# Kernel tuning notes

Hardware: AMD Instinct MI355X
Metric: run time of the kernel (lower is better)

Reference implementation:

```python
import jax, jax.numpy as jnp
import numpy as np

NUM_HEADS = 8
DIM = 256
NUM_Q = 1


def setup_inputs() -> dict:
    key = jax.random.key(0)
    ks = jax.random.split(key, 10)
    B, H, W, C = 4, 56, 56, DIM
    mask_h = mask_w = 7
    WinNum = mask_h * mask_w
    x = jax.random.normal(ks[0], (B, H, W, C), dtype=jnp.float32)
    clstoken = jax.random.normal(ks[1], (B, NUM_Q, C), dtype=jnp.float32)
    mask = jax.random.bernoulli(ks[2], 0.3, (B, WinNum, WinNum))
    # ensure each window attends to itself (avoid fully-masked rows)
    eye = jnp.eye(WinNum, dtype=bool)[None]
    mask = jnp.logical_or(mask, eye)
    Wqkv = jax.random.normal(ks[3], (C, 3 * C), dtype=jnp.float32) * (C ** -0.5)
    bqkv = jnp.zeros((3 * C,), dtype=jnp.float32)
    Wo = jax.random.normal(ks[4], (C, C), dtype=jnp.float32) * (C ** -0.5)
    bo = jnp.zeros((C,), dtype=jnp.float32)
    lepe_k = jax.random.normal(ks[5], (3, 3, 1, C), dtype=jnp.float32) * 0.1  # depthwise HWIO
    lepe_b = jnp.zeros((C,), dtype=jnp.float32)
    return {"x": x, "clstoken": clstoken, "mask": mask, "mask_h": mask_h,
            "mask_w": mask_w, "Wqkv": Wqkv, "bqkv": bqkv, "Wo": Wo, "bo": bo,
            "lepe_k": lepe_k, "lepe_b": lepe_b}


def _forward(x, clstoken, mask, mask_h, mask_w, Wqkv, bqkv, Wo, bo, lepe_k, lepe_b):
    B, H, W, C = x.shape
    num_q = clstoken.shape[1]
    Nh = NUM_HEADS
    Hd = C // Nh
    Win_h, Win_w = H // mask_h, W // mask_w
    WinPix = Win_h * Win_w
    WinNum = mask_h * mask_w
    L_win = H * W
    scale = C ** -0.5

    qkv = x @ Wqkv + bqkv                       # [B,H,W,3C]
    q, k, v = jnp.split(qkv, 3, axis=-1)
    qkv_cls = clstoken @ Wqkv + bqkv            # [B,Q,3C]
    q_cls, k_cls, v_cls = jnp.split(qkv_cls, 3, axis=-1)

    # depthwise lepe conv on v (NHWC)
    lepe = jax.lax.conv_general_dilated(
        v, lepe_k, window_strides=(1, 1), padding='SAME',
        dimension_numbers=('NHWC', 'HWIO', 'NHWC'), feature_group_count=C) + lepe_b

    def to_win(t):  # b (j h)(i w)(Nh Hd) -> b Nh (j i h w) Hd
        t = t.reshape(B, mask_h, Win_h, mask_w, Win_w, Nh, Hd)
        t = t.transpose(0, 5, 1, 3, 2, 4, 6)
        return t.reshape(B, Nh, L_win, Hd)

    def cls_heads(t):  # b q (Nh Hd) -> b Nh q Hd
        return t.reshape(B, num_q, Nh, Hd).transpose(0, 2, 1, 3)

    q_all = jnp.concatenate([to_win(q), cls_heads(q_cls)], axis=2)
    k_all = jnp.concatenate([to_win(k), cls_heads(k_cls)], axis=2)
    v_all = jnp.concatenate([to_win(v), cls_heads(v_cls)], axis=2)

    # token-level block mask; cls block (id WinNum) is globally visible
    blk = jnp.concatenate([jnp.arange(L_win) // WinPix,
                           jnp.full((num_q,), WinNum)])
    mask_ext = jnp.pad(mask, ((0, 0), (0, 1), (0, 1)), constant_values=True)
    tok_mask = mask_ext[:, blk[:, None], blk[None, :]]  # [B,L,L]

    scores = jnp.einsum('bnqd,bnkd->bnqk', q_all, k_all) * scale
    neg = jnp.finfo(scores.dtype).min
    scores = jnp.where(tok_mask[:, None], scores, neg)
    attn = jax.nn.softmax(scores, axis=-1)
    out = jnp.einsum('bnqk,bnkd->bnqd', attn, v_all)   # [B,Nh,L,Hd]

    cls_out = out[:, :, -num_q:, :]
    x_out = out[:, :, :-num_q, :]
    # b Nh (j i h w) Hd -> b (j h)(i w)(Nh Hd)
    x_out = x_out.reshape(B, Nh, mask_h, mask_w, Win_h, Win_w, Hd)
    x_out = x_out.transpose(0, 2, 4, 3, 5, 1, 6).reshape(B, H, W, C)
    cls_out = cls_out.transpose(0, 2, 1, 3).reshape(B, num_q, C)

    x_out = (x_out + lepe) @ Wo + bo
    cls_out = cls_out @ Wo + bo
    return x_out, cls_out


def reference(x, clstoken, mask, mask_h, mask_w, Wqkv, bqkv, Wo, bo, lepe_k, lepe_b):
    return _forward(x, clstoken, mask, mask_h, mask_w, Wqkv, bqkv, Wo, bo, lepe_k, lepe_b)
```

## Files before the change

kernel.cpp:

```cpp
#include <hip/hip_runtime.h>
#include <math.h>

#define B_      4
#define NH      8
#define HD      32
#define WINNUM  49
#define LWIN    3136
#define NTOK    3137
#define NPIX    12544
#define MROWS   12548
#define SCALE_L2E 0.09016844005556021f
#define SM_BIAS   4.0f

typedef _Float16 half_t;
using half8 = __attribute__((ext_vector_type(8))) half_t;
using half4 = __attribute__((ext_vector_type(4))) half_t;
using f32x4 = __attribute__((ext_vector_type(4))) float;

__device__ __forceinline__ unsigned pack2(float a, float b) {
    auto h = __builtin_amdgcn_cvt_pkrtz(a, b);
    return __builtin_bit_cast(unsigned, h);
}
__device__ __forceinline__ half8 as_h8(int4 v) {
    return __builtin_bit_cast(half8, v);
}

__global__ __launch_bounds__(256)
void prep(const float* __restrict__ x, const float* __restrict__ cls,
          const float* __restrict__ Wqkv, const float* __restrict__ Wo,
          half_t* __restrict__ xh, half_t* __restrict__ Wqkvt, half_t* __restrict__ Wot)
{
    const int idx = blockIdx.x * 256 + threadIdx.x;
    const int stride = gridDim.x * 256;
    for (int i = idx; i < MROWS * 256; i += stride) {
        int row = i >> 8, c = i & 255;
        float v = (row < NPIX) ? x[i] : cls[(row - NPIX) * 256 + c];
        xh[i] = (half_t)v;
    }
    for (int i = idx; i < 768 * 256; i += stride) {
        int n = i >> 8, k = i & 255;
        Wqkvt[i] = (half_t)Wqkv[k * 768 + n];
    }
    for (int i = idx; i < 256 * 256; i += stride) {
        int n = i >> 8, k = i & 255;
        Wot[i] = (half_t)Wo[k * 256 + n];
    }
}

__global__ __launch_bounds__(256)
void qkv_gemm(const half_t* __restrict__ xh, const half_t* __restrict__ Bt,
              const float* __restrict__ bqkv,
              half_t* __restrict__ qh, half_t* __restrict__ kh,
              half_t* __restrict__ khcls, half_t* __restrict__ vh,
              half_t* __restrict__ vplain)
{
    __shared__ __align__(16) short As[2][128 * 40];
    __shared__ __align__(16) short Bs[2][128 * 40];
    const int m0 = blockIdx.y * 128, n0 = blockIdx.x * 128;
    const int tid = threadIdx.x;
    const int lane = tid & 63, wv = tid >> 6;
    const int wm = wv >> 1, wn = wv & 1;
    const int qi = lane & 15, g = lane >> 4;
    f32x4 acc[4][4] = {};

    int4 ra[2], rb[2];
    auto issue = [&](int k0) {
#pragma unroll
        for (int i = 0; i < 2; ++i) {
            int ch = tid + 256 * i;
            int row = ch >> 2, kc = (ch & 3) * 8;
            int m = m0 + row;
            ra[i] = (m < MROWS) ? *(const int4*)(xh + (size_t)m * 256 + k0 + kc)
                                : make_int4(0, 0, 0, 0);
            rb[i] = *(const int4*)(Bt + (size_t)(n0 + row) * 256 + k0 + kc);
        }
    };
    auto commit = [&](int bu) {
#pragma unroll
        for (int i = 0; i < 2; ++i) {
            int ch = tid + 256 * i;
            int row = ch >> 2, kc = (ch & 3) * 8;
            *(int4*)&As[bu][row * 40 + kc] = ra[i];
            *(int4*)&Bs[bu][row * 40 + kc] = rb[i];
        }
    };

    issue(0); commit(0);
    __syncthreads();
    int buf = 0;
    for (int s = 0; s < 8; ++s) {
        if (s < 7) issue((s + 1) * 32);
        half8 af[4], bf[4];
#pragma unroll
        for (int f = 0; f < 4; ++f) {
            af[f] = *(const half8*)&As[buf][(wm * 64 + f * 16 + qi) * 40 + g * 8];
            bf[f] = *(const half8*)&Bs[buf][(wn * 64 + f * 16 + qi) * 40 + g * 8];
        }
#pragma unroll
        for (int fm = 0; fm < 4; ++fm)
#pragma unroll
            for (int fn = 0; fn < 4; ++fn)
                acc[fm][fn] = __builtin_amdgcn_mfma_f32_16x16x32_f16(af[fm], bf[fn], acc[fm][fn], 0, 0, 0);
        if (s < 7) commit(buf ^ 1);
        __syncthreads();
        buf ^= 1;
    }

    const int part = n0 >> 8;
    int nhv[4], dv[4];
    float bq[4];
#pragma unroll
    for (int fn = 0; fn < 4; ++fn) {
        int n = n0 + wn * 64 + fn * 16 + qi;
        bq[fn] = bqkv[n];
        int c = n & 255;
        nhv[fn] = c >> 5; dv[fn] = c & 31;
    }
#pragma unroll
    for (int fm = 0; fm < 4; ++fm) {
#pragma unroll
        for (int r = 0; r < 4; ++r) {
            int m = m0 + wm * 64 + fm * 16 + g * 4 + r;
            if (m >= MROWS) continue;
            int b, tok;
            if (m < NPIX) {
                b = m / LWIN;
                int p = m - b * LWIN;
                int hh = p / 56, ww = p - hh * 56;
                tok = ((hh >> 3) * 7 + (ww >> 3)) * 64 + ((hh & 7) << 3) + (ww & 7);
            } else { b = m - NPIX; tok = LWIN; }
#pragma unroll
            for (int fn = 0; fn < 4; ++fn) {
                float val = acc[fm][fn][r] + bq[fn];
                size_t bh = (size_t)(b * NH + nhv[fn]);
                int d = dv[fn];
                if (part == 0) {
                    qh[(bh * NTOK + tok) * 32 + d] = (half_t)(val * SCALE_L2E);
                } else if (part == 1) {
                    if (tok < LWIN) kh[(bh * WINNUM + (tok >> 6)) * 2560 + (tok & 63) * 40 + d] = (half_t)val;
                    else            khcls[bh * 32 + d] = (half_t)val;
                } else {
                    vplain[(bh * NTOK + tok) * 32 + d] = (half_t)val;
                    if (tok < LWIN) vh[(bh * WINNUM + (tok >> 6)) * 2560 + d * 80 + (tok & 63)] = (half_t)val;
                }
            }
        }
    }
}

__global__ __launch_bounds__(256)
void win_attn(const half_t* __restrict__ qh, const half_t* __restrict__ kh,
              const half_t* __restrict__ khcls, const half_t* __restrict__ vh,
              const half_t* __restrict__ vplain, const int* __restrict__ mask,
              half_t* __restrict__ tg, float* __restrict__ clspart)
{
    const int id = blockIdx.x;
    const int tid = threadIdx.x;
    __shared__ __align__(16) short Plds[4][16 * 72];
    __shared__ float redc[4 * 33];
    const int lane = tid & 63, wv = tid >> 6;

    if (id >= 1568) {
        const int cid = id - 1568;
        const int bh = cid >> 3;
        const int chunk = cid & 7;
        const int wstart = chunk * 6;
        const int nw = (chunk < 7) ? 6 : 7;
        const int nkeys = nw * 64;

        float q[32];
        {
            const half_t* qp = qh + ((size_t)bh * NTOK + LWIN) * 32;
#pragma unroll
            for (int d = 0; d < 32; ++d) q[d] = (float)qp[d];
        }
        float l = 0.f, o[32];
#pragma unroll
        for (int d = 0; d < 32; ++d) o[d] = 0.f;

        const half_t* kwb = kh + (size_t)bh * (WINNUM * 2560) + wstart * 2560;
        const half_t* vb  = vplain + ((size_t)bh * NTOK + wstart * 64) * 32;

        for (int kk = tid; kk < nkeys; kk += 256) {
            const half_t* kp = kwb + (kk >> 6) * 2560 + (kk & 63) * 40;
            float s = 0.f;
#pragma unroll
            for (int c8 = 0; c8 < 4; ++c8) {
                half8 kv = *(const half8*)(kp + c8 * 8);
#pragma unroll
                for (int j = 0; j < 8; ++j) s += q[c8 * 8 + j] * (float)kv[j];
            }
            float pp = exp2f(s - SM_BIAS);
            l += pp;
            const half_t* vp = vb + (size_t)kk * 32;
#pragma unroll
            for (int c8 = 0; c8 < 4; ++c8) {
                half8 vvv = *(const half8*)(vp + c8 * 8);
#pragma unroll
                for (int j = 0; j < 8; ++j) o[c8 * 8 + j] += pp * (float)vvv[j];
            }
        }
        if (chunk == 7 && tid == 0) {
            const half_t* kp = khcls + bh * 32;
            float s = 0.f;
#pragma unroll
            for (int d = 0; d < 32; ++d) s += q[d] * (float)kp[d];
            float pp = exp2f(s - SM_BIAS);
            l += pp;
            const half_t* vp = vplain + ((size_t)bh * NTOK + LWIN) * 32;
#pragma unroll
            for (int d = 0; d < 32; ++d) o[d] += pp * (float)vp[d];
        }
#pragma unroll
        for (int off = 1; off < 64; off <<= 1) {
            l += __shfl_xor(l, off);
#pragma unroll
            for (int d = 0; d < 32; ++d) o[d] += __shfl_xor(o[d], off);
        }
        if (lane == 0) {
#pragma unroll
            for (int d = 0; d < 32; ++d) redc[wv * 33 + d] = o[d];
            redc[wv * 33 + 32] = l;
        }
        __syncthreads();
        if (tid < 33) {
            float s = redc[tid] + redc[33 + tid] + redc[66 + tid] + redc[99 + tid];
            clspart[(bh * 8 + chunk) * 33 + tid] = s;
        }
        return;
    }

    const int sw = (id & 7) * 196 + (id >> 3);
    const int wi = sw % 49;
    const int bh = sw / 49;
    const int b = bh >> 3, nh = bh & 7;

    const int g = lane >> 4, qi = lane & 15;
    const int qrow = wi * 64 + wv * 16 + qi;

    half8 aq = *(const half8*)(qh + ((size_t)bh * NTOK + qrow) * 32 + g * 8);

    float lacc = 0.f;
    f32x4 acc[2] = {{0.f,0.f,0.f,0.f},{0.f,0.f,0.f,0.f}};

    const int* mrow = mask + (b * WINNUM + wi) * WINNUM;
    int mv = (lane < WINNUM) ? mrow[lane] : 0;
    unsigned long long rem = __ballot(mv != 0);

    const half_t* kwin = kh + (size_t)bh * (WINNUM * 2560);
    const half_t* vwin = vh + (size_t)bh * (WINNUM * 2560);
    const int koff = qi * 40 + g * 8;
    const int voff = qi * 80 + g * 8;

    short* pw = &Plds[wv][qi * 72];
    const short* prd = &Plds[wv][qi * 72 + g * 8];

    while (rem) {
        const int wj = __builtin_ctzll(rem);
        rem &= rem - 1;
        const half_t* kb = kwin + wj * 2560 + koff;
        const half_t* vb = vwin + wj * 2560 + voff;
        int4 kf0 = *(const int4*)(kb);
        int4 kf1 = *(const int4*)(kb + 640);
        int4 kf2 = *(const int4*)(kb + 1280);
        int4 kf3 = *(const int4*)(kb + 1920);
        int4 vf00 = *(const int4*)(vb);
        int4 vf01 = *(const int4*)(vb + 32);
        int4 vf10 = *(const int4*)(vb + 1280);
        int4 vf11 = *(const int4*)(vb + 1312);

        f32x4 st[4];
        __builtin_amdgcn_s_setprio(1);
        st[0] = __builtin_amdgcn_mfma_f32_16x16x32_f16(as_h8(kf0), aq, (f32x4){0.f,0.f,0.f,0.f}, 0, 0, 0);
        st[1] = __builtin_amdgcn_mfma_f32_16x16x32_f16(as_h8(kf1), aq, (f32x4){0.f,0.f,0.f,0.f}, 0, 0, 0);
        st[2] = __builtin_amdgcn_mfma_f32_16x16x32_f16(as_h8(kf2), aq, (f32x4){0.f,0.f,0.f,0.f}, 0, 0, 0);
        st[3] = __builtin_amdgcn_mfma_f32_16x16x32_f16(as_h8(kf3), aq, (f32x4){0.f,0.f,0.f,0.f}, 0, 0, 0);
        __builtin_amdgcn_s_setprio(0);

#pragma unroll
        for (int t = 0; t < 4; ++t) {
            float p0 = exp2f(st[t][0] - SM_BIAS);
            float p1 = exp2f(st[t][1] - SM_BIAS);
            float p2 = exp2f(st[t][2] - SM_BIAS);
            float p3 = exp2f(st[t][3] - SM_BIAS);
            lacc += (p0 + p1) + (p2 + p3);
            uint2 pk = make_uint2(pack2(p0, p1), pack2(p2, p3));
            *(uint2*)&pw[t * 16 + 4 * g] = pk;
        }
        half8 bp0 = *(const half8*)(prd);
        half8 bp1 = *(const half8*)(prd + 32);
        __builtin_amdgcn_s_setprio(1);
        acc[0] = __builtin_amdgcn_mfma_f32_16x16x32_f16(as_h8(vf00), bp0, acc[0], 0, 0, 0);
        acc[1] = __builtin_amdgcn_mfma_f32_16x16x32_f16(as_h8(vf10), bp0, acc[1], 0, 0, 0);
        acc[0] = __builtin_amdgcn_mfma_f32_16x16x32_f16(as_h8(vf01), bp1, acc[0], 0, 0, 0);
        acc[1] = __builtin_amdgcn_mfma_f32_16x16x32_f16(as_h8(vf11), bp1, acc[1], 0, 0, 0);
        __builtin_amdgcn_s_setprio(0);
    }

    lacc += __shfl_xor(lacc, 16);
    lacc += __shfl_xor(lacc, 32);

    float kcls[8], vcls[2][4];
#pragma unroll
    for (int j = 0; j < 8; ++j) kcls[j] = (float)khcls[bh * 32 + g * 8 + j];
    {
        const half_t* vcb = vplain + ((size_t)bh * NTOK + LWIN) * 32;
#pragma unroll
        for (int h2 = 0; h2 < 2; ++h2)
#pragma unroll
            for (int r = 0; r < 4; ++r) vcls[h2][r] = (float)vcb[h2 * 16 + g * 4 + r];
    }
    float sc = 0.f;
#pragma unroll
    for (int j = 0; j < 8; ++j) sc += (float)aq[j] * kcls[j];
    sc += __shfl_xor(sc, 16);
    sc += __shfl_xor(sc, 32);
    float pc = exp2f(sc - SM_BIAS);
    float l = lacc + pc;
#pragma unroll
    for (int h2 = 0; h2 < 2; ++h2)
#pragma unroll
        for (int r = 0; r < 4; ++r) acc[h2][r] += pc * vcls[h2][r];

    {
        float inv = 1.f / l;
        int kk = wv * 16 + qi;
        int hh = (wi / 7) * 8 + (kk >> 3);
        int ww = (wi % 7) * 8 + (kk & 7);
        size_t pix = (size_t)b * LWIN + hh * 56 + ww;
        half_t* tp = tg + pix * 256 + nh * 32;
#pragma unroll
        for (int h2 = 0; h2 < 2; ++h2) {
            half4 hv;
#pragma unroll
            for (int r = 0; r < 4; ++r) hv[r] = (half_t)(acc[h2][r] * inv);
            *(half4*)(tp + h2 * 16 + g * 4) = hv;
        }
    }
}

__global__ __launch_bounds__(256)
void lepe_add(const half_t* __restrict__ vplain, const float* __restrict__ lk,
              const float* __restrict__ lb, const float* __restrict__ clspart,
              half_t* __restrict__ tg)
{
    if (blockIdx.x == 1568) {
        const int c = threadIdx.x;
        const int nh = c >> 5, d = c & 31;
#pragma unroll
        for (int b = 0; b < 4; ++b) {
            int bh = b * NH + nh;
            float os = 0.f, ls = 0.f;
#pragma unroll
            for (int ch = 0; ch < 8; ++ch) {
                os += clspart[(bh * 8 + ch) * 33 + d];
                ls += clspart[(bh * 8 + ch) * 33 + 32];
            }
            tg[(size_t)(NPIX + b) * 256 + c] = (half_t)(os / ls);
        }
        return;
    }
    const int gidx = blockIdx.x * 256 + threadIdx.x;
    const int pix = gidx >> 5, cg = gidx & 31;
    const int c0 = cg * 8;
    const int b = pix / LWIN, p = pix - b * LWIN;
    const int hh = p / 56, ww = p - hh * 56;
    const int nh = c0 >> 5, d0 = c0 & 31;
    const half_t* vb = vplain + (size_t)(b * NH + nh) * NTOK * 32 + d0;

    float s[8];
#pragma unroll
    for (int j = 0; j < 8; ++j) s[j] = lb[c0 + j];
#pragma unroll
    for (int dh = -1; dh <= 1; ++dh) {
        int hn = hh + dh;
        if (hn < 0 || hn >= 56) continue;
#pragma unroll
        for (int dw = -1; dw <= 1; ++dw) {
            int wn = ww + dw;
            if (wn < 0 || wn >= 56) continue;
            int tok = ((hn >> 3) * 7 + (wn >> 3)) * 64 + ((hn & 7) << 3) + (wn & 7);
            half8 vvv = *(const half8*)(vb + (size_t)tok * 32);
            const float* kk = lk + ((dh + 1) * 3 + (dw + 1)) * 256 + c0;
#pragma unroll
            for (int j = 0; j < 8; ++j) s[j] += (float)vvv[j] * kk[j];
        }
    }
    half_t* tp = tg + (size_t)pix * 256 + c0;
    half8 cur = *(const half8*)tp;
    half8 outv;
#pragma unroll
    for (int j = 0; j < 8; ++j) outv[j] = (half_t)((float)cur[j] + s[j]);
    *(half8*)tp = outv;
}

__global__ __launch_bounds__(256)
void out_gemm(const half_t* __restrict__ th, const half_t* __restrict__ Bt,
              const float* __restrict__ bo, float* __restrict__ out)
{
    __shared__ __align__(16) short As[2][128 * 40];
    __shared__ __align__(16) short Bs[2][128 * 40];
    const int m0 = blockIdx.y * 128, n0 = blockIdx.x * 128;
    const int tid = threadIdx.x;
    const int lane = tid & 63, wv = tid >> 6;
    const int wm = wv >> 1, wn = wv & 1;
    const int qi = lane & 15, g = lane >> 4;
    f32x4 acc[4][4] = {};

    int4 ra[2], rb[2];
    auto issue = [&](int k0) {
#pragma unroll
        for (int i = 0; i < 2; ++i) {
            int ch = tid + 256 * i;
            int row = ch >> 2, kc = (ch & 3) * 8;
            int m = m0 + row;
            ra[i] = (m < MROWS) ? *(const int4*)(th + (size_t)m * 256 + k0 + kc)
                                : make_int4(0, 0, 0, 0);
            rb[i] = *(const int4*)(Bt + (size_t)(n0 + row) * 256 + k0 + kc);
        }
    };
    auto commit = [&](int bu) {
#pragma unroll
        for (int i = 0; i < 2; ++i) {
            int ch = tid + 256 * i;
            int row = ch >> 2, kc = (ch & 3) * 8;
            *(int4*)&As[bu][row * 40 + kc] = ra[i];
            *(int4*)&Bs[bu][row * 40 + kc] = rb[i];
        }
    };

    issue(0); commit(0);
    __syncthreads();
    int buf = 0;
    for (int s = 0; s < 8; ++s) {
        if (s < 7) issue((s + 1) * 32);
        half8 af[4], bf[4];
#pragma unroll
        for (int f = 0; f < 4; ++f) {
            af[f] = *(const half8*)&As[buf][(wm * 64 + f * 16 + qi) * 40 + g * 8];
            bf[f] = *(const half8*)&Bs[buf][(wn * 64 + f * 16 + qi) * 40 + g * 8];
        }
#pragma unroll
        for (int fm = 0; fm < 4; ++fm)
#pragma unroll
            for (int fn = 0; fn < 4; ++fn)
                acc[fm][fn] = __builtin_amdgcn_mfma_f32_16x16x32_f16(af[fm], bf[fn], acc[fm][fn], 0, 0, 0);
        if (s < 7) commit(buf ^ 1);
        __syncthreads();
        buf ^= 1;
    }

    float bov[4];
    int nn[4];
#pragma unroll
    for (int fn = 0; fn < 4; ++fn) {
        nn[fn] = n0 + wn * 64 + fn * 16 + qi;
        bov[fn] = bo[nn[fn]];
    }
#pragma unroll
    for (int fm = 0; fm < 4; ++fm)
#pragma unroll
        for (int r = 0; r < 4; ++r) {
            int m = m0 + wm * 64 + fm * 16 + g * 4 + r;
            if (m >= MROWS) continue;
#pragma unroll
            for (int fn = 0; fn < 4; ++fn)
                out[(size_t)m * 256 + nn[fn]] = acc[fm][fn][r] + bov[fn];
        }
}

extern "C" void kernel_launch(void* const* d_in, const int* in_sizes, int n_in,
                              void* d_out, int out_size, void* d_ws, size_t ws_size,
                              hipStream_t stream)
{
    const float* x    = (const float*)d_in[0];
    const float* cls  = (const float*)d_in[1];
    const int*   mask = (const int*)d_in[2];
    const float* Wqkv = (const float*)d_in[5];
    const float* bqkv = (const float*)d_in[6];
    const float* Wo   = (const float*)d_in[7];
    const float* bo   = (const float*)d_in[8];
    const float* lk   = (const float*)d_in[9];
    const float* lb   = (const float*)d_in[10];
    float* out = (float*)d_out;

    char* w = (char*)d_ws;
    half_t* xh     = (half_t*)w;  w += 6424576;
    half_t* qh     = (half_t*)w;  w += 6424576;
    half_t* kh     = (half_t*)w;  w += 8028160;
    half_t* khcls  = (half_t*)w;  w += 2048;
    half_t* vh     = (half_t*)w;  w += 8028160;
    half_t* vplain = (half_t*)w;  w += 6424576;
    half_t* Wqkvt  = (half_t*)w;  w += 393216;
    half_t* Wot    = (half_t*)w;  w += 131072;
    half_t* th     = (half_t*)w;  w += 6424576;
    float*  clspart= (float*)w;   w += 33792;

    prep<<<1600, 256, 0, stream>>>(x, cls, Wqkv, Wo, xh, Wqkvt, Wot);
    qkv_gemm<<<dim3(6, 99), 256, 0, stream>>>(xh, Wqkvt, bqkv, qh, kh, khcls, vh, vplain);
    win_attn<<<1824, 256, 0, stream>>>(qh, kh, khcls, vh, vplain, mask, th, clspart);
    lepe_add<<<1569, 256, 0, stream>>>(vplain, lk, lb, clspart, th);
    out_gemm<<<dim3(2, 99), 256, 0, stream>>>(th, Wot, bo, out);
}
```

Measured before the change: 122.1 us.

## Fuse x fp16 cast into QKV GEMM, LePE into attention, shrink out-GEMM tile

The separate pass that casts x to fp16 is removed; the QKV GEMM now loads fp32 x and cls directly and packs them to fp16 when writing to LDS. The LePE depthwise conv is folded into the window attention epilogue, which removes the lepe_add kernel and its read-modify-write of the intermediate buffer, leaving a tiny cls_norm kernel. Softmax row sums now come from an extra MFMA against a ones fragment instead of scalar adds plus shuffles, and the SM_BIAS offset is dropped, which raises fp16 overflow risk in the packed probabilities. The output GEMM uses 64-row tiles to roughly double the block count; the LePE conv now accumulates in fp16.

```diff
diff --git a/kernel.cpp b/kernel.cpp
--- a/kernel.cpp
+++ b/kernel.cpp
@@ -10,7 +10,6 @@
 #define NPIX    12544
 #define MROWS   12548
 #define SCALE_L2E 0.09016844005556021f
-#define SM_BIAS   4.0f
 
 typedef _Float16 half_t;
 using half8 = __attribute__((ext_vector_type(8))) half_t;
@@ -26,17 +25,13 @@
 }
 
 __global__ __launch_bounds__(256)
-void prep(const float* __restrict__ x, const float* __restrict__ cls,
-          const float* __restrict__ Wqkv, const float* __restrict__ Wo,
-          half_t* __restrict__ xh, half_t* __restrict__ Wqkvt, half_t* __restrict__ Wot)
+void prep(const float* __restrict__ Wqkv, const float* __restrict__ Wo,
+          const float* __restrict__ lk, const float* __restrict__ lb,
+          half_t* __restrict__ Wqkvt, half_t* __restrict__ Wot,
+          half_t* __restrict__ lkh, half_t* __restrict__ lbh)
 {
     const int idx = blockIdx.x * 256 + threadIdx.x;
     const int stride = gridDim.x * 256;
-    for (int i = idx; i < MROWS * 256; i += stride) {
-        int row = i >> 8, c = i & 255;
-        float v = (row < NPIX) ? x[i] : cls[(row - NPIX) * 256 + c];
-        xh[i] = (half_t)v;
-    }
     for (int i = idx; i < 768 * 256; i += stride) {
         int n = i >> 8, k = i & 255;
         Wqkvt[i] = (half_t)Wqkv[k * 768 + n];
@@ -45,11 +40,13 @@
         int n = i >> 8, k = i & 255;
         Wot[i] = (half_t)Wo[k * 256 + n];
     }
+    for (int i = idx; i < 9 * 256; i += stride) lkh[i] = (half_t)lk[i];
+    for (int i = idx; i < 256; i += stride) lbh[i] = (half_t)lb[i];
 }
 
 __global__ __launch_bounds__(256)
-void qkv_gemm(const half_t* __restrict__ xh, const half_t* __restrict__ Bt,
-              const float* __restrict__ bqkv,
+void qkv_gemm(const float* __restrict__ x, const float* __restrict__ cls,
+              const half_t* __restrict__ Bt, const float* __restrict__ bqkv,
               half_t* __restrict__ qh, half_t* __restrict__ kh,
               half_t* __restrict__ khcls, half_t* __restrict__ vh,
               half_t* __restrict__ vplain)
@@ -63,15 +60,22 @@
     const int qi = lane & 15, g = lane >> 4;
     f32x4 acc[4][4] = {};
 
-    int4 ra[2], rb[2];
+    float4 rfa[2][2];
+    int4 rb[2];
     auto issue = [&](int k0) {
 #pragma unroll
         for (int i = 0; i < 2; ++i) {
             int ch = tid + 256 * i;
             int row = ch >> 2, kc = (ch & 3) * 8;
             int m = m0 + row;
-            ra[i] = (m < MROWS) ? *(const int4*)(xh + (size_t)m * 256 + k0 + kc)
-                                : make_int4(0, 0, 0, 0);
+            if (m < MROWS) {
+                const float* src = ((m < NPIX) ? (x + (size_t)m * 256)
+                                               : (cls + (size_t)(m - NPIX) * 256)) + k0 + kc;
+                rfa[i][0] = *(const float4*)src;
+                rfa[i][1] = *(const float4*)(src + 4);
+            } else {
+                rfa[i][0] = rfa[i][1] = make_float4(0.f, 0.f, 0.f, 0.f);
+            }
             rb[i] = *(const int4*)(Bt + (size_t)(n0 + row) * 256 + k0 + kc);
         }
     };
@@ -80,7 +84,9 @@
         for (int i = 0; i < 2; ++i) {
             int ch = tid + 256 * i;
             int row = ch >> 2, kc = (ch & 3) * 8;
-            *(int4*)&As[bu][row * 40 + kc] = ra[i];
+            uint4 pa = make_uint4(pack2(rfa[i][0].x, rfa[i][0].y), pack2(rfa[i][0].z, rfa[i][0].w),
+                                  pack2(rfa[i][1].x, rfa[i][1].y), pack2(rfa[i][1].z, rfa[i][1].w));
+            *(uint4*)&As[bu][row * 40 + kc] = pa;
             *(int4*)&Bs[bu][row * 40 + kc] = rb[i];
         }
     };
@@ -152,6 +158,7 @@
 void win_attn(const half_t* __restrict__ qh, const half_t* __restrict__ kh,
               const half_t* __restrict__ khcls, const half_t* __restrict__ vh,
               const half_t* __restrict__ vplain, const int* __restrict__ mask,
+              const half_t* __restrict__ lkh, const half_t* __restrict__ lbh,
               half_t* __restrict__ tg, float* __restrict__ clspart)
 {
     const int id = blockIdx.x;
@@ -190,7 +197,7 @@
 #pragma unroll
                 for (int j = 0; j < 8; ++j) s += q[c8 * 8 + j] * (float)kv[j];
             }
-            float pp = exp2f(s - SM_BIAS);
+            float pp = exp2f(s);
             l += pp;
             const half_t* vp = vb + (size_t)kk * 32;
 #pragma unroll
@@ -205,7 +212,7 @@
             float s = 0.f;
 #pragma unroll
             for (int d = 0; d < 32; ++d) s += q[d] * (float)kp[d];
-            float pp = exp2f(s - SM_BIAS);
+            float pp = exp2f(s);
             l += pp;
             const half_t* vp = vplain + ((size_t)bh * NTOK + LWIN) * 32;
 #pragma unroll
@@ -240,8 +247,14 @@
 
     half8 aq = *(const half8*)(qh + ((size_t)bh * NTOK + qrow) * 32 + g * 8);
 
-    float lacc = 0.f;
+    half8 onesA = {};
+    if (qi == 0) {
+#pragma unroll
+        for (int j = 0; j < 8; ++j) onesA[j] = (half_t)1.0f;
+    }
+
     f32x4 acc[2] = {{0.f,0.f,0.f,0.f},{0.f,0.f,0.f,0.f}};
+    f32x4 acc_l = {0.f,0.f,0.f,0.f};
 
     const int* mrow = mask + (b * WINNUM + wi) * WINNUM;
     int mv = (lane < WINNUM) ? mrow[lane] : 0;
@@ -279,11 +292,10 @@
 
 #pragma unroll
         for (int t = 0; t < 4; ++t) {
-            float p0 = exp2f(st[t][0] - SM_BIAS);
-            float p1 = exp2f(st[t][1] - SM_BIAS);
-            float p2 = exp2f(st[t][2] - SM_BIAS);
-            float p3 = exp2f(st[t][3] - SM_BIAS);
-            lacc += (p0 + p1) + (p2 + p3);
+            float p0 = exp2f(st[t][0]);
+            float p1 = exp2f(st[t][1]);
+            float p2 = exp2f(st[t][2]);
+            float p3 = exp2f(st[t][3]);
             uint2 pk = make_uint2(pack2(p0, p1), pack2(p2, p3));
             *(uint2*)&pw[t * 16 + 4 * g] = pk;
         }
@@ -292,13 +304,14 @@
         __builtin_amdgcn_s_setprio(1);
         acc[0] = __builtin_amdgcn_mfma_f32_16x16x32_f16(as_h8(vf00), bp0, acc[0], 0, 0, 0);
         acc[1] = __builtin_amdgcn_mfma_f32_16x16x32_f16(as_h8(vf10), bp0, acc[1], 0, 0, 0);
+        acc_l  = __builtin_amdgcn_mfma_f32_16x16x32_f16(onesA, bp0, acc_l, 0, 0, 0);
         acc[0] = __builtin_amdgcn_mfma_f32_16x16x32_f16(as_h8(vf01), bp1, acc[0], 0, 0, 0);
         acc[1] = __builtin_amdgcn_mfma_f32_16x16x32_f16(as_h8(vf11), bp1, acc[1], 0, 0, 0);
+        acc_l  = __builtin_amdgcn_mfma_f32_16x16x32_f16(onesA, bp1, acc_l, 0, 0, 0);
         __builtin_amdgcn_s_setprio(0);
     }
 
-    lacc += __shfl_xor(lacc, 16);
-    lacc += __shfl_xor(lacc, 32);
+    float lwin = __shfl(acc_l[0], qi);
 
     float kcls[8], vcls[2][4];
 #pragma unroll
@@ -315,116 +328,113 @@
     for (int j = 0; j < 8; ++j) sc += (float)aq[j] * kcls[j];
     sc += __shfl_xor(sc, 16);
     sc += __shfl_xor(sc, 32);
-    float pc = exp2f(sc - SM_BIAS);
-    float l = lacc + pc;
+    float pc = exp2f(sc);
+    float l = lwin + pc;
 #pragma unroll
     for (int h2 = 0; h2 < 2; ++h2)
 #pragma unroll
         for (int r = 0; r < 4; ++r) acc[h2][r] += pc * vcls[h2][r];
+
+    const int kk = wv * 16 + qi;
+    const int hh = (wi / 7) * 8 + (kk >> 3);
+    const int ww = (wi % 7) * 8 + (kk & 7);
+    const int c0 = nh * 32;
+    half4 conv[2];
+    conv[0] = *(const half4*)(lbh + c0 + g * 4);
+    conv[1] = *(const half4*)(lbh + c0 + 16 + g * 4);
+    {
+        const half_t* vpb = vplain + (size_t)bh * NTOK * 32 + g * 4;
+#pragma unroll
+        for (int dh = -1; dh <= 1; ++dh) {
+            int hn = hh + dh;
+            if (hn < 0 || hn >= 56) continue;
+#pragma unroll
+            for (int dw = -1; dw <= 1; ++dw) {
+                int wn = ww + dw;
+                if (wn < 0 || wn >= 56) continue;
+                int tok2 = ((hn >> 3) * 7 + (wn >> 3)) * 64 + ((hn & 7) << 3) + (wn & 7);
+                int tap = (dh + 1) * 3 + (dw + 1);
+                const half_t* vp = vpb + (size_t)tok2 * 32;
+                half4 v0 = *(const half4*)(vp);
+                half4 v1 = *(const half4*)(vp + 16);
+                half4 k0 = *(const half4*)(lkh + tap * 256 + c0 + g * 4);
+                half4 k1 = *(const half4*)(lkh + tap * 256 + c0 + 16 + g * 4);
+                conv[0] += v0 * k0;
+                conv[1] += v1 * k1;
+            }
+        }
+    }
 
     {
         float inv = 1.f / l;
-        int kk = wv * 16 + qi;
-        int hh = (wi / 7) * 8 + (kk >> 3);
-        int ww = (wi % 7) * 8 + (kk & 7);
         size_t pix = (size_t)b * LWIN + hh * 56 + ww;
         half_t* tp = tg + pix * 256 + nh * 32;
 #pragma unroll
         for (int h2 = 0; h2 < 2; ++h2) {
             half4 hv;
 #pragma unroll
-            for (int r = 0; r < 4; ++r) hv[r] = (half_t)(acc[h2][r] * inv);
+            for (int r = 0; r < 4; ++r)
+                hv[r] = (half_t)(acc[h2][r] * inv + (float)conv[h2][r]);
             *(half4*)(tp + h2 * 16 + g * 4) = hv;
         }
     }
 }
 
 __global__ __launch_bounds__(256)
-void lepe_add(const half_t* __restrict__ vplain, const float* __restrict__ lk,
-              const float* __restrict__ lb, const float* __restrict__ clspart,
-              half_t* __restrict__ tg)
+void cls_norm(const float* __restrict__ clspart, half_t* __restrict__ tg)
 {
-    if (blockIdx.x == 1568) {
-        const int c = threadIdx.x;
-        const int nh = c >> 5, d = c & 31;
-#pragma unroll
-        for (int b = 0; b < 4; ++b) {
-            int bh = b * NH + nh;
-            float os = 0.f, ls = 0.f;
-#pragma unroll
-            for (int ch = 0; ch < 8; ++ch) {
-                os += clspart[(bh * 8 + ch) * 33 + d];
-                ls += clspart[(bh * 8 + ch) * 33 + 32];
-            }
-            tg[(size_t)(NPIX + b) * 256 + c] = (half_t)(os / ls);
-        }
-        return;
-    }
-    const int gidx = blockIdx.x * 256 + threadIdx.x;
-    const int pix = gidx >> 5, cg = gidx & 31;
-    const int c0 = cg * 8;
-    const int b = pix / LWIN, p = pix - b * LWIN;
-    const int hh = p / 56, ww = p - hh * 56;
-    const int nh = c0 >> 5, d0 = c0 & 31;
-    const half_t* vb = vplain + (size_t)(b * NH + nh) * NTOK * 32 + d0;
-
-    float s[8];
-#pragma unroll
-    for (int j = 0; j < 8; ++j) s[j] = lb[c0 + j];
-#pragma unroll
-    for (int dh = -1; dh <= 1; ++dh) {
-        int hn = hh + dh;
-        if (hn < 0 || hn >= 56) continue;
-#pragma unroll
-        for (int dw = -1; dw <= 1; ++dw) {
-            int wn = ww + dw;
-            if (wn < 0 || wn >= 56) continue;
-            int tok = ((hn >> 3) * 7 + (wn >> 3)) * 64 + ((hn & 7) << 3) + (wn & 7);
-            half8 vvv = *(const half8*)(vb + (size_t)tok * 32);
-            const float* kk = lk + ((dh + 1) * 3 + (dw + 1)) * 256 + c0;
-#pragma unroll
-            for (int j = 0; j < 8; ++j) s[j] += (float)vvv[j] * kk[j];
-        }
-    }
-    half_t* tp = tg + (size_t)pix * 256 + c0;
-    half8 cur = *(const half8*)tp;
-    half8 outv;
-#pragma unroll
-    for (int j = 0; j < 8; ++j) outv[j] = (half_t)((float)cur[j] + s[j]);
-    *(half8*)tp = outv;
+    const int c = threadIdx.x;
+    const int nh = c >> 5, d = c & 31;
+#pragma unroll
+    for (int b = 0; b < 4; ++b) {
+        int bh = b * NH + nh;
+        float os = 0.f, ls = 0.f;
+#pragma unroll
+        for (int ch = 0; ch < 8; ++ch) {
+            os += clspart[(bh * 8 + ch) * 33 + d];
+            ls += clspart[(bh * 8 + ch) * 33 + 32];
+        }
+        tg[(size_t)(NPIX + b) * 256 + c] = (half_t)(os / ls);
+    }
 }
 
 __global__ __launch_bounds__(256)
 void out_gemm(const half_t* __restrict__ th, const half_t* __restrict__ Bt,
               const float* __restrict__ bo, float* __restrict__ out)
 {
-    __shared__ __align__(16) short As[2][128 * 40];
+    __shared__ __align__(16) short As[2][64 * 40];
     __shared__ __align__(16) short Bs[2][128 * 40];
-    const int m0 = blockIdx.y * 128, n0 = blockIdx.x * 128;
+    const int m0 = blockIdx.y * 64, n0 = blockIdx.x * 128;
     const int tid = threadIdx.x;
     const int lane = tid & 63, wv = tid >> 6;
     const int wm = wv >> 1, wn = wv & 1;
     const int qi = lane & 15, g = lane >> 4;
-    f32x4 acc[4][4] = {};
-
-    int4 ra[2], rb[2];
+    f32x4 acc[2][4] = {};
+
+    int4 ra, rb[2];
     auto issue = [&](int k0) {
+        {
+            int row = tid >> 2, kc = (tid & 3) * 8;
+            int m = m0 + row;
+            ra = (m < MROWS) ? *(const int4*)(th + (size_t)m * 256 + k0 + kc)
+                             : make_int4(0, 0, 0, 0);
+        }
 #pragma unroll
         for (int i = 0; i < 2; ++i) {
             int ch = tid + 256 * i;
             int row = ch >> 2, kc = (ch & 3) * 8;
-            int m = m0 + row;
-            ra[i] = (m < MROWS) ? *(const int4*)(th + (size_t)m * 256 + k0 + kc)
-                                : make_int4(0, 0, 0, 0);
             rb[i] = *(const int4*)(Bt + (size_t)(n0 + row) * 256 + k0 + kc);
         }
     };
     auto commit = [&](int bu) {
+        {
+            int row = tid >> 2, kc = (tid & 3) * 8;
+            *(int4*)&As[bu][row * 40 + kc] = ra;
+        }
 #pragma unroll
         for (int i = 0; i < 2; ++i) {
             int ch = tid + 256 * i;
             int row = ch >> 2, kc = (ch & 3) * 8;
-            *(int4*)&As[bu][row * 40 + kc] = ra[i];
             *(int4*)&Bs[bu][row * 40 + kc] = rb[i];
         }
     };
@@ -434,14 +444,15 @@
     int buf = 0;
     for (int s = 0; s < 8; ++s) {
         if (s < 7) issue((s + 1) * 32);
-        half8 af[4], bf[4];
-#pragma unroll
-        for (int f = 0; f < 4; ++f) {
-            af[f] = *(const half8*)&As[buf][(wm * 64 + f * 16 + qi) * 40 + g * 8];
+        half8 af[2], bf[4];
+#pragma unroll
+        for (int f = 0; f < 2; ++f)
+            af[f] = *(const half8*)&As[buf][(wm * 32 + f * 16 + qi) * 40 + g * 8];
+#pragma unroll
+        for (int f = 0; f < 4; ++f)
             bf[f] = *(const half8*)&Bs[buf][(wn * 64 + f * 16 + qi) * 40 + g * 8];
-        }
-#pragma unroll
-        for (int fm = 0; fm < 4; ++fm)
+#pragma unroll
+        for (int fm = 0; fm < 2; ++fm)
 #pragma unroll
             for (int fn = 0; fn < 4; ++fn)
                 acc[fm][fn] = __builtin_amdgcn_mfma_f32_16x16x32_f16(af[fm], bf[fn], acc[fm][fn], 0, 0, 0);
@@ -458,10 +469,10 @@
         bov[fn] = bo[nn[fn]];
     }
 #pragma unroll
-    for (int fm = 0; fm < 4; ++fm)
+    for (int fm = 0; fm < 2; ++fm)
 #pragma unroll
         for (int r = 0; r < 4; ++r) {
-            int m = m0 + wm * 64 + fm * 16 + g * 4 + r;
+            int m = m0 + wm * 32 + fm * 16 + g * 4 + r;
             if (m >= MROWS) continue;
 #pragma unroll
             for (int fn = 0; fn < 4; ++fn)
@@ -485,7 +496,6 @@
     float* out = (float*)d_out;
 
     char* w = (char*)d_ws;
-    half_t* xh     = (half_t*)w;  w += 6424576;
     half_t* qh     = (half_t*)w;  w += 6424576;
     half_t* kh     = (half_t*)w;  w += 8028160;
     half_t* khcls  = (half_t*)w;  w += 2048;
@@ -495,10 +505,12 @@
     half_t* Wot    = (half_t*)w;  w += 131072;
     half_t* th     = (half_t*)w;  w += 6424576;
     float*  clspart= (float*)w;   w += 33792;
-
-    prep<<<1600, 256, 0, stream>>>(x, cls, Wqkv, Wo, xh, Wqkvt, Wot);
-    qkv_gemm<<<dim3(6, 99), 256, 0, stream>>>(xh, Wqkvt, bqkv, qh, kh, khcls, vh, vplain);
-    win_attn<<<1824, 256, 0, stream>>>(qh, kh, khcls, vh, vplain, mask, th, clspart);
-    lepe_add<<<1569, 256, 0, stream>>>(vplain, lk, lb, clspart, th);
-    out_gemm<<<dim3(2, 99), 256, 0, stream>>>(th, Wot, bo, out);
-}
+    half_t* lkh    = (half_t*)w;  w += 4608;
+    half_t* lbh    = (half_t*)w;  w += 512;
+
+    prep<<<256, 256, 0, stream>>>(Wqkv, Wo, lk, lb, Wqkvt, Wot, lkh, lbh);
+    qkv_gemm<<<dim3(6, 99), 256, 0, stream>>>(x, cls, Wqkvt, bqkv, qh, kh, khcls, vh, vplain);
+    win_attn<<<1824, 256, 0, stream>>>(qh, kh, khcls, vh, vplain, mask, lkh, lbh, th, clspart);
+    cls_norm<<<1, 256, 0, stream>>>(clspart, th);
+    out_gemm<<<dim3(2, 197), 256, 0, stream>>>(th, Wot, bo, out);
+}
```

After: 124.2 us. No clear change (+1.7%).
